# Performance work log

Measured on AMD Instinct MI355X. Metric: run time of the kernel, lower is better.

Reference implementation:

```python
import jax, jax.numpy as jnp
import numpy as np

# Kernel codes matching style 'L;O2;P2;Y2,1,1;R0.5;W1,1'
KERNEL_CODES = ['L', 'O', 'P', 'Y', 'R', 'W']
SM_TEMP = 1.0


def _norm_sq(q, k):
    # q: [n,l,h,e], k: [n,s,h,e] -> [n,h,l,s]
    q2 = jnp.einsum('nlhe,nlhe->nhl', q, q)[..., None]        # [n,h,l,1]
    k2 = jnp.einsum('nshe,nshe->nhs', k, k)[:, :, None, :]     # [n,h,1,s]
    qk = jnp.einsum('nlhe,nshe->nhls', q, k)
    return q2 + k2 - 2.0 * qk


def _kernel(code, q, k):
    if code == 'L':
        return jnp.einsum('nlhe,nshe->nhls', q, k)
    if code == 'O':  # -log(1 + ns^(p/2)), p=2
        return -jnp.log1p(_norm_sq(q, k))
    if code == 'P':  # -(ns)^(p/2), p=2
        return -_norm_sq(q, k)
    if code == 'Y':  # (alpha*<q,k> + c)^p, p=2, alpha=1, c=1
        d = jnp.einsum('nlhe,nshe->nhls', q, k)
        return (d + 1.0) ** 2
    if code == 'R':  # exp(-gamma*ns), gamma=0.5
        return jnp.exp(-0.5 * _norm_sq(q, k))
    if code == 'W':  # cos(ns/a)*exp(-ns/b), a=b=1
        ns = _norm_sq(q, k)
        return jnp.cos(ns) * jnp.exp(-ns)
    raise ValueError(code)


def setup_inputs() -> dict:
    key = jax.random.key(0)
    k1, k2, k3, k4 = jax.random.split(key, 4)
    N, L, S, H, E, K = 2, 1024, 1024, 8, 64, 6
    return {
        'query': jax.random.normal(k1, (N, L, H, E), dtype=jnp.float32),
        'key': jax.random.normal(k2, (N, S, H, E), dtype=jnp.float32),
        'attn_mask_add': jnp.zeros((N, L, S), dtype=jnp.float32),
        'key_lengths_add': jnp.zeros((N, S), dtype=jnp.float32),
        'M': jax.random.uniform(k3, (H, E, K), dtype=jnp.float32),
        'C': jax.random.uniform(k4, (K, H, E, E), dtype=jnp.float32),
    }


def reference(query, key, attn_mask_add, key_lengths_add, M, C):
    # mixture weights pi: [n,l,h,k]
    pi = jax.nn.softmax(jnp.einsum('nlhe,hek->nlhk', query, M), axis=-1)
    out = None
    for c, code in enumerate(KERNEL_CODES):
        # htilde = tanh(query @ C[c]): [n,l,h,e]
        htilde = jnp.tanh(jnp.einsum('nlhe,hef->nlhf', query, C[c]))
        qk = _kernel(code, htilde, key)                    # [n,h,l,s]
        qk = qk + attn_mask_add[:, None] + key_lengths_add[:, None, None, :]
        sm = jax.nn.softmax(SM_TEMP * qk, axis=-1)
        w = jnp.transpose(pi[..., c], (0, 2, 1))[..., None]  # [n,h,l,1]
        term = sm * w
        out = term if out is None else out + term
    return out
```

## Files before the change

### kernel.cpp

```cpp
#include <hip/hip_runtime.h>
#include <hip/hip_bf16.h>
#include <math.h>

#define N_  2
#define H_  8
#define G_  16
#define L_  1024
#define S_  1024
#define E_  64
#define NC_ 6

typedef __attribute__((ext_vector_type(4))) float floatx4;
typedef __attribute__((ext_vector_type(8))) short short8;

#define MFMA16 __builtin_amdgcn_mfma_f32_16x16x32_bf16

#define AHAT_OFF   0
#define AHAT_BYTES (NC_*G_*L_*128*2)
#define KHAT_OFF   (AHAT_OFF + AHAT_BYTES)
#define KHAT_BYTES (G_*S_*128*2)
#define PI_OFF     (KHAT_OFF + KHAT_BYTES)
#define PI_BYTES   (NC_*G_*L_*4)
#define HSQ_OFF    (PI_OFF + PI_BYTES)
#define HSQ_BYTES  (NC_*G_*L_*4)
#define KSQ_OFF    (HSQ_OFF + HSQ_BYTES)
#define KSQ_BYTES  (G_*S_*4)

__device__ __forceinline__ float ftanh(float x) {
  return 1.0f - 2.0f * __builtin_amdgcn_rcpf(__expf(2.0f*x) + 1.0f);
}

__global__ __launch_bounds__(256) void k_htilde(
    const float* __restrict__ q, const float* __restrict__ C,
    __hip_bfloat16* __restrict__ Ahat, float* __restrict__ hsq) {
  extern __shared__ char smraw[];
  float* qs = (float*)smraw;
  float* Cs = qs + 128*68;

  const int lch = blockIdx.x, c = blockIdx.y, g = blockIdx.z;
  const int n = g >> 3, h = g & 7;
  const int l0 = lch * 128;
  const int t = threadIdx.x;

  for (int u = t; u < 2048; u += 256) {
    int row = u >> 4, seg = u & 15;
    *(float4*)(qs + row*68 + seg*4) =
      *(const float4*)(q + (((size_t)(n*L_ + l0 + row))*H_ + h)*E_ + seg*4);
  }
  for (int u = t; u < 1024; u += 256) {
    int e = u >> 4, seg = u & 15;
    *(float4*)(Cs + e*68 + seg*4) =
      *(const float4*)(C + (((size_t)(c*8 + h))*64 + e)*64 + seg*4);
  }
  __syncthreads();

  const int rg = t >> 3, fg = t & 7;
  float acc[4][8];
  #pragma unroll
  for (int i = 0; i < 4; i++)
    #pragma unroll
    for (int j = 0; j < 8; j++) acc[i][j] = 0.0f;

  #pragma unroll 4
  for (int e0 = 0; e0 < 64; e0 += 4) {
    float4 q4[4];
    #pragma unroll
    for (int i = 0; i < 4; i++)
      q4[i] = *(const float4*)(qs + (rg*4 + i)*68 + e0);
    #pragma unroll
    for (int ee = 0; ee < 4; ee++) {
      float4 ca = *(const float4*)(Cs + (e0+ee)*68 + fg*8);
      float4 cb = *(const float4*)(Cs + (e0+ee)*68 + fg*8 + 4);
      float c8[8] = {ca.x, ca.y, ca.z, ca.w, cb.x, cb.y, cb.z, cb.w};
      #pragma unroll
      for (int i = 0; i < 4; i++) {
        float qv = (ee == 0) ? q4[i].x : (ee == 1) ? q4[i].y
                 : (ee == 2) ? q4[i].z : q4[i].w;
        #pragma unroll
        for (int j = 0; j < 8; j++) acc[i][j] = fmaf(qv, c8[j], acc[i][j]);
      }
    }
  }

  #pragma unroll
  for (int i = 0; i < 4; i++) {
    int l = l0 + rg*4 + i;
    size_t rowb = (((size_t)(c*G_ + g))*L_ + l) * 128;
    float ss = 0.0f;
    short8 hi8, lo8;
    #pragma unroll
    for (int j = 0; j < 8; j++) {
      float hv = ftanh(acc[i][j]);
      ss += hv*hv;
      __hip_bfloat16 hi = __float2bfloat16(hv);
      __hip_bfloat16 lo = __float2bfloat16(hv - __bfloat162float(hi));
      short hs, ls;
      __builtin_memcpy(&hs, &hi, 2);
      __builtin_memcpy(&ls, &lo, 2);
      hi8[j] = hs; lo8[j] = ls;
    }
    *(short8*)((char*)Ahat + (rowb + fg*8)*2)      = hi8;
    *(short8*)((char*)Ahat + (rowb + 64 + fg*8)*2) = lo8;
    ss += __shfl_xor(ss, 1); ss += __shfl_xor(ss, 2); ss += __shfl_xor(ss, 4);
    if (fg == 0) hsq[((size_t)(c*G_ + g))*L_ + l] = ss;
  }
}

__global__ __launch_bounds__(256) void k_pi(
    const float* __restrict__ q, const float* __restrict__ M,
    float* __restrict__ pi_t) {
  __shared__ float Ms[384];
  const int g = blockIdx.x >> 2, lch = blockIdx.x & 3;
  const int n = g >> 3, h = g & 7;
  const int t = threadIdx.x;
  const int l = lch*256 + t;
  for (int u = t; u < 384; u += 256) Ms[u] = M[h*384 + u];
  __syncthreads();
  const float* qrow = q + (((size_t)(n*L_ + l))*H_ + h)*E_;
  float p[6] = {0.f, 0.f, 0.f, 0.f, 0.f, 0.f};
  #pragma unroll 8
  for (int e = 0; e < 64; e++) {
    float qv = qrow[e];
    #pragma unroll
    for (int k = 0; k < 6; k++) p[k] = fmaf(qv, Ms[e*6 + k], p[k]);
  }
  float mx = p[0];
  #pragma unroll
  for (int k = 1; k < 6; k++) mx = fmaxf(mx, p[k]);
  float den = 0.f;
  #pragma unroll
  for (int k = 0; k < 6; k++) den += __expf(p[k] - mx);
  float rden = __builtin_amdgcn_rcpf(den);
  #pragma unroll
  for (int k = 0; k < 6; k++)
    pi_t[((size_t)(k*G_ + g))*L_ + l] = __expf(p[k] - mx) * rden;
}

__global__ __launch_bounds__(256) void k_key(
    const float* __restrict__ key, __hip_bfloat16* __restrict__ Khat,
    float* __restrict__ ksq) {
  int t = threadIdx.x; int wv = t >> 6; int lane = t & 63;
  int r = blockIdx.x*4 + wv;
  int g = r >> 10; int s = r & 1023; int n = g >> 3; int h = g & 7;
  float v = key[(((size_t)(n*S_ + s))*H_ + h)*E_ + lane];
  __hip_bfloat16 hi = __float2bfloat16(v);
  __hip_bfloat16 lo = __float2bfloat16(v - __bfloat162float(hi));
  size_t base = ((size_t)g*S_ + s)*128;
  Khat[base + lane]      = hi;
  Khat[base + 64 + lane] = lo;
  float sq = v*v;
  #pragma unroll
  for (int off = 32; off; off >>= 1) sq += __shfl_xor(sq, off);
  if (lane == 0) ksq[(size_t)g*S_ + s] = sq;
}

#define LDS_ZRED  0
#define LDS_MRED  1536
#define LDS_CST   3072
#define LDS_TOTAL 3840

__global__ __launch_bounds__(256, 2) void k_main(
    const __hip_bfloat16* __restrict__ Ahat, const __hip_bfloat16* __restrict__ Khat,
    const float* __restrict__ hsq, const float* __restrict__ ksq,
    const float* __restrict__ mask, const float* __restrict__ klen,
    const float* __restrict__ pi_t, float* __restrict__ out) {
  extern __shared__ char smraw[];
  float*  zred   = (float*)(smraw + LDS_ZRED);
  float*  mred   = (float*)(smraw + LDS_MRED);
  float2* cst    = (float2*)(smraw + LDS_CST);

  const int l0 = blockIdx.x * 16; const int g = blockIdx.y; const int n = g >> 3;
  const int t = threadIdx.x; const int w = t >> 6; const int lane = t & 63;
  const int quad = lane >> 4; const int lc = lane & 15;

  short8 a6f[6][4];
  #pragma unroll
  for (int cc = 0; cc < 6; cc++)
    #pragma unroll
    for (int kt = 0; kt < 4; kt++)
      a6f[cc][kt] = *(const short8*)((const char*)Ahat +
          (((size_t)(cc*G_ + g))*L_ + l0 + lc)*256 + kt*64 + quad*16);

  float h1p[4], nh2[4], h4h[4], nh5[4];
  #pragma unroll
  for (int i = 0; i < 4; i++) {
    int r = quad*4 + i;
    h1p[i] = 1.0f + hsq[((size_t)(1*G_ + g))*L_ + l0 + r];
    nh2[i] = 64.0f - hsq[((size_t)(2*G_ + g))*L_ + l0 + r];
    h4h[i] = -0.5f * hsq[((size_t)(4*G_ + g))*L_ + l0 + r];
    nh5[i] = -hsq[((size_t)(5*G_ + g))*L_ + l0 + r];
  }

  float Zc[4][4], zp[4], m3[4], z3[4];
  #pragma unroll
  for (int i = 0; i < 4; i++) {
    #pragma unroll
    for (int c = 0; c < 4; c++) Zc[c][i] = 0.0f;
    zp[i] = 0.0f; m3[i] = -INFINITY; z3[i] = 0.0f;
  }

  #pragma unroll 1
  for (int st = 0; st < 16; st++) {
    int s0 = st*64;
    int scol = s0 + w*16 + lc;
    short8 bfr[4];
    #pragma unroll
    for (int kt = 0; kt < 4; kt++)
      bfr[kt] = *(const short8*)((const char*)Khat +
          (((size_t)g)*S_ + scol)*256 + kt*64 + quad*16);
    float kq  = ksq[(size_t)g*S_ + scol];
    float klv = klen[(size_t)n*S_ + scol];
    float mk[4];
    #pragma unroll
    for (int i = 0; i < 4; i++)
      mk[i] = mask[((size_t)(n*L_ + l0 + quad*4 + i))*S_ + scol];
    float mv[4], Ev[4], oc[4], pc[4], rc[4], wc[4];
    #pragma unroll
    for (int i = 0; i < 4; i++) {
      mv[i] = mk[i] + klv;
      Ev[i] = __expf(mv[i]);
      oc[i] = h1p[i] + kq;
      pc[i] = nh2[i] - kq + mv[i];
      rc[i] = fmaf(-0.5f, kq, h4h[i]);
      wc[i] = nh5[i] - kq;
    }
    #pragma unroll
    for (int c = 0; c < 6; c++) {
      floatx4 a = {0.f, 0.f, 0.f, 0.f};
      a = MFMA16(a6f[c][0], bfr[0], a, 0,0,0);
      a = MFMA16(a6f[c][1], bfr[1], a, 0,0,0);
      a = MFMA16(a6f[c][0], bfr[2], a, 0,0,0);
      a = MFMA16(a6f[c][1], bfr[3], a, 0,0,0);
      a = MFMA16(a6f[c][2], bfr[0], a, 0,0,0);
      a = MFMA16(a6f[c][3], bfr[1], a, 0,0,0);
      #pragma unroll
      for (int i = 0; i < 4; i++) {
        float d = a[i];
        if (c == 0) {
          Zc[0][i] = fmaf(Ev[i], __expf(d), Zc[0][i]);
        } else if (c == 1) {
          Zc[1][i] = fmaf(Ev[i], __builtin_amdgcn_rcpf(fmaf(-2.f, d, oc[i])), Zc[1][i]);
        } else if (c == 2) {
          zp[i] += __expf(fmaf(2.f, d, pc[i]));
        } else if (c == 3) {
          float tt = d + 1.f;
          float x  = fmaf(tt, tt, mv[i]);
          float mn = fmaxf(m3[i], x);
          float e  = __expf(fminf(m3[i], x) - mn);
          z3[i] = (x > m3[i]) ? fmaf(z3[i], e, 1.0f) : (z3[i] + e);
          m3[i] = mn;
        } else if (c == 4) {
          Zc[2][i] = fmaf(Ev[i], __expf(__expf(d + rc[i])), Zc[2][i]);
        } else {
          float a5 = fmaf(2.f, d, wc[i]);
          Zc[3][i] = fmaf(Ev[i], __expf(__cosf(a5) * __expf(a5)), Zc[3][i]);
        }
      }
    }
  }

  #pragma unroll
  for (int off = 1; off < 16; off <<= 1) {
    #pragma unroll
    for (int c = 0; c < 4; c++)
      #pragma unroll
      for (int i = 0; i < 4; i++) Zc[c][i] += __shfl_xor(Zc[c][i], off);
    #pragma unroll
    for (int i = 0; i < 4; i++) {
      zp[i] += __shfl_xor(zp[i], off);
      float mo = __shfl_xor(m3[i], off);
      float zo = __shfl_xor(z3[i], off);
      float mn = fmaxf(m3[i], mo);
      float e  = __expf(fminf(m3[i], mo) - mn);
      z3[i] = (mo > m3[i]) ? fmaf(z3[i], e, zo) : fmaf(zo, e, z3[i]);
      m3[i] = mn;
    }
  }
  if (lc == 0) {
    static const int cmap[4] = {0, 1, 4, 5};
    #pragma unroll
    for (int c = 0; c < 4; c++)
      #pragma unroll
      for (int i = 0; i < 4; i++) {
        zred[w*96 + cmap[c]*16 + quad*4 + i] = Zc[c][i];
        mred[w*96 + cmap[c]*16 + quad*4 + i] = 0.f;
      }
    #pragma unroll
    for (int i = 0; i < 4; i++) {
      zred[w*96 + 2*16 + quad*4 + i] = zp[i];
      mred[w*96 + 2*16 + quad*4 + i] = 0.f;
      zred[w*96 + 3*16 + quad*4 + i] = z3[i];
      mred[w*96 + 3*16 + quad*4 + i] = m3[i];
    }
  }
  __syncthreads();
  if (t < 96) {
    int c = t >> 4;
    float z = zred[t], m = mred[t];
    if (c == 3) {
      #pragma unroll
      for (int w2 = 1; w2 < 4; w2++) {
        float mo = mred[w2*96 + t], zo = zred[w2*96 + t];
        float mn = fmaxf(m, mo);
        float e  = __expf(fminf(m, mo) - mn);
        z = (mo > m) ? fmaf(z, e, zo) : fmaf(zo, e, z);
        m = mn;
      }
    } else {
      #pragma unroll
      for (int w2 = 1; w2 < 4; w2++) z += zred[w2*96 + t];
    }
    float piv = pi_t[((size_t)((t >> 4)*G_ + g))*L_ + l0 + (t & 15)];
    cst[t] = make_float2(piv / z, m);
  }
  __syncthreads();

  float ac[6][4], m3f[4];
  #pragma unroll
  for (int c = 0; c < 6; c++)
    #pragma unroll
    for (int i = 0; i < 4; i++) {
      float2 v = cst[c*16 + quad*4 + i];
      ac[c][i] = v.x;
      if (c == 3) m3f[i] = v.y;
    }

  #pragma unroll 1
  for (int st = 0; st < 16; st++) {
    int s0 = st*64;
    int scol = s0 + w*16 + lc;
    short8 bfr[4];
    #pragma unroll
    for (int kt = 0; kt < 4; kt++)
      bfr[kt] = *(const short8*)((const char*)Khat +
          (((size_t)g)*S_ + scol)*256 + kt*64 + quad*16);
    float kq  = ksq[(size_t)g*S_ + scol];
    float klv = klen[(size_t)n*S_ + scol];
    float mk[4];
    #pragma unroll
    for (int i = 0; i < 4; i++)
      mk[i] = mask[((size_t)(n*L_ + l0 + quad*4 + i))*S_ + scol];
    float mv[4], Ev[4], oc[4], pc[4], rc[4], wc[4];
    #pragma unroll
    for (int i = 0; i < 4; i++) {
      mv[i] = mk[i] + klv;
      Ev[i] = __expf(mv[i]);
      oc[i] = h1p[i] + kq;
      pc[i] = nh2[i] - kq + mv[i];
      rc[i] = fmaf(-0.5f, kq, h4h[i]);
      wc[i] = nh5[i] - kq;
    }
    float Sacc[4] = {0.f, 0.f, 0.f, 0.f};
    float G[4]    = {0.f, 0.f, 0.f, 0.f};
    #pragma unroll
    for (int c = 0; c < 6; c++) {
      floatx4 a = {0.f, 0.f, 0.f, 0.f};
      a = MFMA16(a6f[c][0], bfr[0], a, 0,0,0);
      a = MFMA16(a6f[c][1], bfr[1], a, 0,0,0);
      a = MFMA16(a6f[c][0], bfr[2], a, 0,0,0);
      a = MFMA16(a6f[c][1], bfr[3], a, 0,0,0);
      a = MFMA16(a6f[c][2], bfr[0], a, 0,0,0);
      a = MFMA16(a6f[c][3], bfr[1], a, 0,0,0);
      #pragma unroll
      for (int i = 0; i < 4; i++) {
        float d = a[i];
        if (c == 0) {
          Sacc[i] = fmaf(ac[0][i], __expf(d), Sacc[i]);
        } else if (c == 1) {
          Sacc[i] = fmaf(ac[1][i], __builtin_amdgcn_rcpf(fmaf(-2.f, d, oc[i])), Sacc[i]);
        } else if (c == 2) {
          G[i] = fmaf(ac[2][i], __expf(fmaf(2.f, d, pc[i])), G[i]);
        } else if (c == 3) {
          float tt = d + 1.f;
          float x  = fmaf(tt, tt, mv[i]);
          G[i] = fmaf(ac[3][i], __expf(x - m3f[i]), G[i]);
        } else if (c == 4) {
          Sacc[i] = fmaf(ac[4][i], __expf(__expf(d + rc[i])), Sacc[i]);
        } else {
          float a5 = fmaf(2.f, d, wc[i]);
          Sacc[i] = fmaf(ac[5][i], __expf(__cosf(a5) * __expf(a5)), Sacc[i]);
        }
      }
    }
    #pragma unroll
    for (int i = 0; i < 4; i++)
      out[(((size_t)g)*L_ + l0 + quad*4 + i)*S_ + scol] = fmaf(Ev[i], Sacc[i], G[i]);
  }
}

extern "C" void kernel_launch(void* const* d_in, const int* in_sizes, int n_in,
                              void* d_out, int out_size, void* d_ws, size_t ws_size,
                              hipStream_t stream) {
  (void)in_sizes; (void)n_in; (void)out_size; (void)ws_size;
  const float* q    = (const float*)d_in[0];
  const float* key  = (const float*)d_in[1];
  const float* mask = (const float*)d_in[2];
  const float* klen = (const float*)d_in[3];
  const float* M    = (const float*)d_in[4];
  const float* C    = (const float*)d_in[5];
  char* ws = (char*)d_ws;
  __hip_bfloat16* Ahat = (__hip_bfloat16*)(ws + AHAT_OFF);
  __hip_bfloat16* Khat = (__hip_bfloat16*)(ws + KHAT_OFF);
  float* pi_t    = (float*)(ws + PI_OFF);
  float* hsq     = (float*)(ws + HSQ_OFF);
  float* ksq     = (float*)(ws + KSQ_OFF);
  float* out = (float*)d_out;

  k_htilde<<<dim3(8, 6, 16), 256, 52224, stream>>>(q, C, Ahat, hsq);
  k_key<<<4096, 256, 0, stream>>>(key, Khat, ksq);
  k_pi<<<64, 256, 0, stream>>>(q, M, pi_t);
  k_main<<<dim3(64, 16), 256, LDS_TOTAL, stream>>>(Ahat, Khat, hsq, ksq, mask, klen,
                                                   pi_t, out);
}
```

Before: 226.7 us.

## Stage A fragments in LDS and double-buffer K tile loads in both sweeps

Moves the six per-kernel A fragments out of registers into a padded LDS tile that is re-read per kernel code, which frees VGPRs. Both S sweeps now software-pipeline the Khat fragment loads with two register buffers, prefetching the next tile while the current tile's MFMAs and transcendentals run. Per-column constants are recomputed inline rather than held in arrays to cut register pressure. The cost is extra LDS reads per MFMA group and a larger LDS footprint per block, which could limit occupancy.

New measurement: 218.5 us. -3.6%, faster.

```diff
diff --git a/kernel.cpp b/kernel.cpp
--- a/kernel.cpp
+++ b/kernel.cpp
@@ -154,10 +154,11 @@
   if (lane == 0) ksq[(size_t)g*S_ + s] = sq;
 }
 
-#define LDS_ZRED  0
-#define LDS_MRED  1536
-#define LDS_CST   3072
-#define LDS_TOTAL 3840
+#define LDS_A6    0
+#define LDS_ZRED  26112
+#define LDS_MRED  27648
+#define LDS_CST   29184
+#define LDS_TOTAL 29952
 
 __global__ __launch_bounds__(256, 2) void k_main(
     const __hip_bfloat16* __restrict__ Ahat, const __hip_bfloat16* __restrict__ Khat,
@@ -165,6 +166,7 @@
     const float* __restrict__ mask, const float* __restrict__ klen,
     const float* __restrict__ pi_t, float* __restrict__ out) {
   extern __shared__ char smraw[];
+  char*   A6     = smraw + LDS_A6;
   float*  zred   = (float*)(smraw + LDS_ZRED);
   float*  mred   = (float*)(smraw + LDS_MRED);
   float2* cst    = (float2*)(smraw + LDS_CST);
@@ -173,13 +175,14 @@
   const int t = threadIdx.x; const int w = t >> 6; const int lane = t & 63;
   const int quad = lane >> 4; const int lc = lane & 15;
 
-  short8 a6f[6][4];
-  #pragma unroll
-  for (int cc = 0; cc < 6; cc++)
-    #pragma unroll
-    for (int kt = 0; kt < 4; kt++)
-      a6f[cc][kt] = *(const short8*)((const char*)Ahat +
-          (((size_t)(cc*G_ + g))*L_ + l0 + lc)*256 + kt*64 + quad*16);
+  #pragma unroll
+  for (int rep = 0; rep < 6; rep++) {
+    int u = t + rep*256; int row = u >> 4, seg = u & 15;
+    int cc = row >> 4, lr = row & 15;
+    *(int4*)(A6 + row*272 + seg*16) =
+      *(const int4*)((const char*)Ahat + (((size_t)(cc*G_ + g))*L_ + l0 + lr)*256 + seg*16);
+  }
+  __syncthreads();
 
   float h1p[4], nh2[4], h4h[4], nh5[4];
   #pragma unroll
@@ -191,6 +194,14 @@
     nh5[i] = -hsq[((size_t)(5*G_ + g))*L_ + l0 + r];
   }
 
+  auto LOADB = [&](int st, short8 (&bf)[4]) {
+    const char* base = (const char*)Khat +
+        (((size_t)g)*S_ + st*64 + w*16 + lc)*256 + quad*16;
+    #pragma unroll
+    for (int kt = 0; kt < 4; kt++)
+      bf[kt] = *(const short8*)(base + kt*64);
+  };
+
   float Zc[4][4], zp[4], m3[4], z3[4];
   #pragma unroll
   for (int i = 0; i < 4; i++) {
@@ -199,49 +210,39 @@
     zp[i] = 0.0f; m3[i] = -INFINITY; z3[i] = 0.0f;
   }
 
-  #pragma unroll 1
-  for (int st = 0; st < 16; st++) {
-    int s0 = st*64;
-    int scol = s0 + w*16 + lc;
-    short8 bfr[4];
-    #pragma unroll
-    for (int kt = 0; kt < 4; kt++)
-      bfr[kt] = *(const short8*)((const char*)Khat +
-          (((size_t)g)*S_ + scol)*256 + kt*64 + quad*16);
+  auto SWEEP1 = [&](int st, const short8 (&bf)[4]) {
+    int scol = st*64 + w*16 + lc;
     float kq  = ksq[(size_t)g*S_ + scol];
     float klv = klen[(size_t)n*S_ + scol];
-    float mk[4];
-    #pragma unroll
-    for (int i = 0; i < 4; i++)
-      mk[i] = mask[((size_t)(n*L_ + l0 + quad*4 + i))*S_ + scol];
-    float mv[4], Ev[4], oc[4], pc[4], rc[4], wc[4];
+    float mv[4], Ev[4];
     #pragma unroll
     for (int i = 0; i < 4; i++) {
-      mv[i] = mk[i] + klv;
+      mv[i] = mask[((size_t)(n*L_ + l0 + quad*4 + i))*S_ + scol] + klv;
       Ev[i] = __expf(mv[i]);
-      oc[i] = h1p[i] + kq;
-      pc[i] = nh2[i] - kq + mv[i];
-      rc[i] = fmaf(-0.5f, kq, h4h[i]);
-      wc[i] = nh5[i] - kq;
     }
     #pragma unroll
     for (int c = 0; c < 6; c++) {
+      short8 af[4];
+      #pragma unroll
+      for (int kt = 0; kt < 4; kt++)
+        af[kt] = *(const short8*)(A6 + (c*16 + lc)*272 + kt*64 + quad*16);
       floatx4 a = {0.f, 0.f, 0.f, 0.f};
-      a = MFMA16(a6f[c][0], bfr[0], a, 0,0,0);
-      a = MFMA16(a6f[c][1], bfr[1], a, 0,0,0);
-      a = MFMA16(a6f[c][0], bfr[2], a, 0,0,0);
-      a = MFMA16(a6f[c][1], bfr[3], a, 0,0,0);
-      a = MFMA16(a6f[c][2], bfr[0], a, 0,0,0);
-      a = MFMA16(a6f[c][3], bfr[1], a, 0,0,0);
+      a = MFMA16(af[0], bf[0], a, 0,0,0);
+      a = MFMA16(af[1], bf[1], a, 0,0,0);
+      a = MFMA16(af[0], bf[2], a, 0,0,0);
+      a = MFMA16(af[1], bf[3], a, 0,0,0);
+      a = MFMA16(af[2], bf[0], a, 0,0,0);
+      a = MFMA16(af[3], bf[1], a, 0,0,0);
       #pragma unroll
       for (int i = 0; i < 4; i++) {
         float d = a[i];
         if (c == 0) {
           Zc[0][i] = fmaf(Ev[i], __expf(d), Zc[0][i]);
         } else if (c == 1) {
-          Zc[1][i] = fmaf(Ev[i], __builtin_amdgcn_rcpf(fmaf(-2.f, d, oc[i])), Zc[1][i]);
+          Zc[1][i] = fmaf(Ev[i],
+              __builtin_amdgcn_rcpf(fmaf(-2.f, d, h1p[i] + kq)), Zc[1][i]);
         } else if (c == 2) {
-          zp[i] += __expf(fmaf(2.f, d, pc[i]));
+          zp[i] += __expf(fmaf(2.f, d, nh2[i] - kq + mv[i]));
         } else if (c == 3) {
           float tt = d + 1.f;
           float x  = fmaf(tt, tt, mv[i]);
@@ -250,12 +251,25 @@
           z3[i] = (x > m3[i]) ? fmaf(z3[i], e, 1.0f) : (z3[i] + e);
           m3[i] = mn;
         } else if (c == 4) {
-          Zc[2][i] = fmaf(Ev[i], __expf(__expf(d + rc[i])), Zc[2][i]);
+          Zc[2][i] = fmaf(Ev[i],
+              __expf(__expf(d + fmaf(-0.5f, kq, h4h[i]))), Zc[2][i]);
         } else {
-          float a5 = fmaf(2.f, d, wc[i]);
+          float a5 = fmaf(2.f, d, nh5[i] - kq);
           Zc[3][i] = fmaf(Ev[i], __expf(__cosf(a5) * __expf(a5)), Zc[3][i]);
         }
       }
+    }
+  };
+
+  {
+    short8 bA[4], bB[4];
+    LOADB(0, bA);
+    #pragma unroll 1
+    for (int st = 0; st < 16; st += 2) {
+      LOADB(st + 1, bB);
+      SWEEP1(st, bA);
+      LOADB((st + 2) & 15, bA);
+      SWEEP1(st + 1, bB);
     }
   }
 
@@ -325,66 +339,69 @@
       if (c == 3) m3f[i] = v.y;
     }
 
-  #pragma unroll 1
-  for (int st = 0; st < 16; st++) {
-    int s0 = st*64;
-    int scol = s0 + w*16 + lc;
-    short8 bfr[4];
-    #pragma unroll
-    for (int kt = 0; kt < 4; kt++)
-      bfr[kt] = *(const short8*)((const char*)Khat +
-          (((size_t)g)*S_ + scol)*256 + kt*64 + quad*16);
+  auto SWEEP2 = [&](int st, const short8 (&bf)[4]) {
+    int scol = st*64 + w*16 + lc;
     float kq  = ksq[(size_t)g*S_ + scol];
     float klv = klen[(size_t)n*S_ + scol];
-    float mk[4];
-    #pragma unroll
-    for (int i = 0; i < 4; i++)
-      mk[i] = mask[((size_t)(n*L_ + l0 + quad*4 + i))*S_ + scol];
-    float mv[4], Ev[4], oc[4], pc[4], rc[4], wc[4];
+    float mv[4], Ev[4];
     #pragma unroll
     for (int i = 0; i < 4; i++) {
-      mv[i] = mk[i] + klv;
+      mv[i] = mask[((size_t)(n*L_ + l0 + quad*4 + i))*S_ + scol] + klv;
       Ev[i] = __expf(mv[i]);
-      oc[i] = h1p[i] + kq;
-      pc[i] = nh2[i] - kq + mv[i];
-      rc[i] = fmaf(-0.5f, kq, h4h[i]);
-      wc[i] = nh5[i] - kq;
     }
     float Sacc[4] = {0.f, 0.f, 0.f, 0.f};
-    float G[4]    = {0.f, 0.f, 0.f, 0.f};
+    float Gg[4]   = {0.f, 0.f, 0.f, 0.f};
     #pragma unroll
     for (int c = 0; c < 6; c++) {
+      short8 af[4];
+      #pragma unroll
+      for (int kt = 0; kt < 4; kt++)
+        af[kt] = *(const short8*)(A6 + (c*16 + lc)*272 + kt*64 + quad*16);
       floatx4 a = {0.f, 0.f, 0.f, 0.f};
-      a = MFMA16(a6f[c][0], bfr[0], a, 0,0,0);
-      a = MFMA16(a6f[c][1], bfr[1], a, 0,0,0);
-      a = MFMA16(a6f[c][0], bfr[2], a, 0,0,0);
-      a = MFMA16(a6f[c][1], bfr[3], a, 0,0,0);
-      a = MFMA16(a6f[c][2], bfr[0], a, 0,0,0);
-      a = MFMA16(a6f[c][3], bfr[1], a, 0,0,0);
+      a = MFMA16(af[0], bf[0], a, 0,0,0);
+      a = MFMA16(af[1], bf[1], a, 0,0,0);
+      a = MFMA16(af[0], bf[2], a, 0,0,0);
+      a = MFMA16(af[1], bf[3], a, 0,0,0);
+      a = MFMA16(af[2], bf[0], a, 0,0,0);
+      a = MFMA16(af[3], bf[1], a, 0,0,0);
       #pragma unroll
       for (int i = 0; i < 4; i++) {
         float d = a[i];
         if (c == 0) {
           Sacc[i] = fmaf(ac[0][i], __expf(d), Sacc[i]);
         } else if (c == 1) {
-          Sacc[i] = fmaf(ac[1][i], __builtin_amdgcn_rcpf(fmaf(-2.f, d, oc[i])), Sacc[i]);
+          Sacc[i] = fmaf(ac[1][i],
+              __builtin_amdgcn_rcpf(fmaf(-2.f, d, h1p[i] + kq)), Sacc[i]);
         } else if (c == 2) {
-          G[i] = fmaf(ac[2][i], __expf(fmaf(2.f, d, pc[i])), G[i]);
+          Gg[i] = fmaf(ac[2][i], __expf(fmaf(2.f, d, nh2[i] - kq + mv[i])), Gg[i]);
         } else if (c == 3) {
           float tt = d + 1.f;
           float x  = fmaf(tt, tt, mv[i]);
-          G[i] = fmaf(ac[3][i], __expf(x - m3f[i]), G[i]);
+          Gg[i] = fmaf(ac[3][i], __expf(x - m3f[i]), Gg[i]);
         } else if (c == 4) {
-          Sacc[i] = fmaf(ac[4][i], __expf(__expf(d + rc[i])), Sacc[i]);
+          Sacc[i] = fmaf(ac[4][i],
+              __expf(__expf(d + fmaf(-0.5f, kq, h4h[i]))), Sacc[i]);
         } else {
-          float a5 = fmaf(2.f, d, wc[i]);
+          float a5 = fmaf(2.f, d, nh5[i] - kq);
           Sacc[i] = fmaf(ac[5][i], __expf(__cosf(a5) * __expf(a5)), Sacc[i]);
         }
       }
     }
     #pragma unroll
     for (int i = 0; i < 4; i++)
-      out[(((size_t)g)*L_ + l0 + quad*4 + i)*S_ + scol] = fmaf(Ev[i], Sacc[i], G[i]);
+      out[(((size_t)g)*L_ + l0 + quad*4 + i)*S_ + scol] = fmaf(Ev[i], Sacc[i], Gg[i]);
+  };
+
+  {
+    short8 bA[4], bB[4];
+    LOADB(0, bA);
+    #pragma unroll 1
+    for (int st = 0; st < 16; st += 2) {
+      LOADB(st + 1, bB);
+      SWEEP2(st, bA);
+      LOADB((st + 2) & 15, bA);
+      SWEEP2(st + 1, bB);
+    }
   }
 }
 
```
